# Performance work log

Measured on AMD Instinct MI355X. Metric: run time of the kernel, lower is better.

Reference implementation:

```python
import jax, jax.numpy as jnp
import numpy as np

T, H, I, E, K = 8192, 2048, 768, 16, 2  # tokens, hidden, moe_intermediate, experts, top_k


def setup_inputs() -> dict:
    key = jax.random.key(0)
    k0, k1, k2, k3, k4 = jax.random.split(key, 5)
    return {
        "hidden_states": jax.random.normal(k0, (T, H), jnp.float32),
        "top_k_index": jax.random.randint(k1, (T, K), 0, E),
        "top_k_weights": jax.random.uniform(k2, (T, K), jnp.float32),
        "gate_up_proj": jax.random.normal(k3, (E, 2 * I, H), jnp.float32) * 0.02,
        "down_proj": jax.random.normal(k4, (E, H, I), jnp.float32) * 0.02,
    }


def reference(hidden_states, top_k_index, top_k_weights, gate_up_proj, down_proj):
    num_experts = gate_up_proj.shape[0]
    # combine[t, e] = sum over k of top_k_weights[t, k] where top_k_index[t, k] == e
    # (duplicated expert picks sum their weights, matching torch index_add_ semantics)
    onehot = jax.nn.one_hot(top_k_index, num_experts, dtype=hidden_states.dtype)  # [T, K, E]
    combine = jnp.einsum("tke,tk->te", onehot, top_k_weights)                      # [T, E]
    out = jnp.zeros_like(hidden_states)
    # fixed small loop over structurally distinct experts; unselected tokens get weight 0
    for e in range(num_experts):
        gate_up = hidden_states @ gate_up_proj[e].T        # [T, 2I]
        gate, up = jnp.split(gate_up, 2, axis=-1)
        act = jax.nn.silu(gate) * up                       # SwiGLU, [T, I]
        down = act @ down_proj[e].T                        # [T, H]
        out = out + down * combine[:, e:e + 1]
    return out
```

## Files before the change

kernel.cpp:

```cpp
#include <hip/hip_runtime.h>

#define TT 8192
#define HH 2048
#define II 768
#define NE 16
#define TOPK 2
#define CAP 16384
#define BM 128

typedef float f32x4 __attribute__((ext_vector_type(4)));
typedef float f32x8 __attribute__((ext_vector_type(8)));
typedef short bf16x8 __attribute__((ext_vector_type(8)));
typedef unsigned short ushort8 __attribute__((ext_vector_type(8)));

__device__ __forceinline__ unsigned short f2bf(float f) {
    unsigned u = __builtin_bit_cast(unsigned, f);
    u += 0x7fffu + ((u >> 16) & 1u);
    return (unsigned short)(u >> 16);
}

__device__ __forceinline__ float bf2f(unsigned short u) {
    return __builtin_bit_cast(float, (unsigned)u << 16);
}

__device__ __forceinline__ void glds16(const void* g, void* l) {
    __builtin_amdgcn_global_load_lds((const __attribute__((address_space(1))) void*)g,
                                     (__attribute__((address_space(3))) void*)l, 16, 0, 0);
}

__global__ void cast_hs_kernel(const float* __restrict__ src, unsigned short* __restrict__ dst) {
    int i = blockIdx.x * blockDim.x + threadIdx.x;
    const float4 v = reinterpret_cast<const float4*>(src)[i];
    ushort4 o;
    o.x = f2bf(v.x); o.y = f2bf(v.y); o.z = f2bf(v.z); o.w = f2bf(v.w);
    reinterpret_cast<ushort4*>(dst)[i] = o;
}

__global__ void cast_w1_kernel(const float* __restrict__ gup, unsigned short* __restrict__ wg1) {
    size_t gid = (size_t)blockIdx.x * 256 + threadIdx.x;
    int sc = gid & 7;
    int r = (gid >> 3) & 255;
    int kt = (gid >> 11) & 31;
    int rest = (int)(gid >> 16);
    int it = rest % 6;
    int e = rest / 6;
    int chunk = sc ^ (r & 7);
    int grow = (r < 128) ? (it * 128 + r) : (II + it * 128 + (r - 128));
    const float4* s = reinterpret_cast<const float4*>(
        &gup[((size_t)e * (2 * II) + grow) * HH + kt * 64 + chunk * 8]);
    float4 v0 = s[0], v1 = s[1];
    ushort8 o;
    o[0] = f2bf(v0.x); o[1] = f2bf(v0.y); o[2] = f2bf(v0.z); o[3] = f2bf(v0.w);
    o[4] = f2bf(v1.x); o[5] = f2bf(v1.y); o[6] = f2bf(v1.z); o[7] = f2bf(v1.w);
    *reinterpret_cast<ushort8*>(&wg1[gid * 8]) = o;
}

__global__ void cast_w2_kernel(const float* __restrict__ dwn, unsigned short* __restrict__ wg2) {
    size_t gid = (size_t)blockIdx.x * 256 + threadIdx.x;
    int sc = gid & 7;
    int r = (gid >> 3) & 127;
    int kt = (int)((gid >> 10) % 12);
    int rest = (int)(gid / (12 << 10));
    int ht = rest & 15;
    int e = rest >> 4;
    int chunk = sc ^ (r & 7);
    int hrow = ht * 128 + r;
    const float4* s = reinterpret_cast<const float4*>(
        &dwn[((size_t)e * HH + hrow) * II + kt * 64 + chunk * 8]);
    float4 v0 = s[0], v1 = s[1];
    ushort8 o;
    o[0] = f2bf(v0.x); o[1] = f2bf(v0.y); o[2] = f2bf(v0.z); o[3] = f2bf(v0.w);
    o[4] = f2bf(v1.x); o[5] = f2bf(v1.y); o[6] = f2bf(v1.z); o[7] = f2bf(v1.w);
    *reinterpret_cast<ushort8*>(&wg2[gid * 8]) = o;
}

__global__ void route_kernel(const int* __restrict__ idx, const float* __restrict__ w,
                             int* __restrict__ counts, int* __restrict__ toks,
                             float* __restrict__ wts) {
    int t = blockIdx.x * blockDim.x + threadIdx.x;
    if (t >= TT) return;
    #pragma unroll
    for (int k = 0; k < TOPK; ++k) {
        int e = idx[t * TOPK + k];
        int p = atomicAdd(&counts[e], 1);
        toks[e * CAP + p] = t | (k << 15);
        wts[e * CAP + p] = w[t * TOPK + k];
    }
}

__global__ void scan_kernel(const int* __restrict__ counts, int* __restrict__ poffs,
                            int* __restrict__ ntot, int* __restrict__ tmap) {
    if (threadIdx.x == 0) {
        int s = 0, nt = 0;
        for (int e = 0; e < NE; ++e) {
            poffs[e] = s;
            int ct = (counts[e] + 127) >> 7;
            for (int m = 0; m < ct; ++m) tmap[nt++] = e | (m << 8);
            s += ct << 7;
        }
        poffs[NE] = s;
        ntot[0] = nt;
    }
}

__global__ __launch_bounds__(256, 2) void gemm1_kernel(
    const unsigned short* __restrict__ hsb, const unsigned short* __restrict__ wg1,
    const int* __restrict__ counts, const int* __restrict__ poffs,
    const int* __restrict__ ntotp, const int* __restrict__ tmap,
    const int* __restrict__ toks, unsigned short* __restrict__ actT) {
    const int b = blockIdx.x;
    const int w = (b & 7) * 108 + (b >> 3);
    const int ibt = w / 144;
    const int gt = w % 144;
    if (gt >= ntotp[0]) return;
    const int ent = tmap[gt];
    const int e = ent & 255;
    const int mbase = (ent >> 8) << 7;
    const int cnt = counts[e];
    const int tid = threadIdx.x;
    const int lane = tid & 63;
    const int wid = tid >> 6;
    const int wm = wid >> 1, wn = wid & 1;

    __shared__ unsigned short sA[128 * 64];
    __shared__ unsigned short sB[256 * 64];
    __shared__ int s_tok[BM];

    if (tid < BM) {
        int r = mbase + tid;
        s_tok[tid] = toks[e * CAP + ((r < cnt) ? r : (cnt - 1))] & 0x1FFF;
    }
    __syncthreads();

    size_t abase[4];
    #pragma unroll
    for (int it = 0; it < 4; ++it) {
        int idx = it * 256 + tid;
        int r = idx >> 3, sc = idx & 7;
        abase[it] = (size_t)s_tok[r] * HH + ((sc ^ (r & 7)) << 3);
    }
    const unsigned short* bbase = wg1 + ((size_t)(e * 6 + ibt) << 19) + (size_t)tid * 8;

    f32x4 accg[4][4], accu[4][4];
    #pragma unroll
    for (int m = 0; m < 4; ++m)
        #pragma unroll
        for (int n = 0; n < 4; ++n) {
            accg[m][n] = (f32x4){0.f, 0.f, 0.f, 0.f};
            accu[m][n] = (f32x4){0.f, 0.f, 0.f, 0.f};
        }

    const int lrow = lane & 15;
    const int lk8 = (lane >> 4) << 3;

    for (int k0 = 0; k0 < HH; k0 += 64) {
        #pragma unroll
        for (int it = 0; it < 4; ++it)
            glds16(hsb + abase[it] + k0, (char*)sA + it * 4096 + wid * 1024);
        const unsigned short* bk = bbase + ((size_t)(k0 >> 6) * 16384);
        #pragma unroll
        for (int it = 0; it < 8; ++it)
            glds16(bk + it * 2048, (char*)sB + it * 4096 + wid * 1024);
        __syncthreads();
        #pragma unroll
        for (int ks = 0; ks < 2; ++ks) {
            bf16x8 af[4], bg[4], bu[4];
            #pragma unroll
            for (int m = 0; m < 4; ++m) {
                int row = wm * 64 + m * 16 + lrow;
                af[m] = *reinterpret_cast<const bf16x8*>(
                    &sA[(row << 6) + ((ks * 32 + lk8) ^ ((row & 7) << 3))]);
            }
            #pragma unroll
            for (int n = 0; n < 4; ++n) {
                int rg = wn * 64 + n * 16 + lrow;
                bg[n] = *reinterpret_cast<const bf16x8*>(
                    &sB[(rg << 6) + ((ks * 32 + lk8) ^ ((rg & 7) << 3))]);
                int ru = rg + 128;
                bu[n] = *reinterpret_cast<const bf16x8*>(
                    &sB[(ru << 6) + ((ks * 32 + lk8) ^ ((ru & 7) << 3))]);
            }
            #pragma unroll
            for (int m = 0; m < 4; ++m)
                #pragma unroll
                for (int n = 0; n < 4; ++n) {
                    accg[m][n] = __builtin_amdgcn_mfma_f32_16x16x32_bf16(af[m], bg[n], accg[m][n], 0, 0, 0);
                    accu[m][n] = __builtin_amdgcn_mfma_f32_16x16x32_bf16(af[m], bu[n], accu[m][n], 0, 0, 0);
                }
        }
        __syncthreads();
    }

    const int mt = (poffs[e] + mbase) >> 7;
    #pragma unroll
    for (int m = 0; m < 4; ++m)
        #pragma unroll
        for (int n = 0; n < 4; ++n)
            #pragma unroll
            for (int j = 0; j < 4; ++j) {
                int row = wm * 64 + m * 16 + ((lane >> 4) << 2) + j;
                if (mbase + row < cnt) {
                    int c = wn * 64 + n * 16 + lrow;
                    int ktile = ibt * 2 + (c >> 6);
                    int cc = c & 63;
                    float g = accg[m][n][j], u = accu[m][n][j];
                    float a = (g / (1.f + __expf(-g))) * u;
                    actT[((size_t)(mt * 12 + ktile) * 128 + row) * 64 +
                         (((cc >> 3) ^ (row & 7)) << 3) + (cc & 7)] = f2bf(a);
                }
            }
}

__global__ __launch_bounds__(256) void gemm2_kernel(
    const unsigned short* __restrict__ actT, const unsigned short* __restrict__ wg2,
    const int* __restrict__ counts, const int* __restrict__ poffs,
    const int* __restrict__ ntotp, const int* __restrict__ tmap,
    const int* __restrict__ toks, const float* __restrict__ wts,
    unsigned short* __restrict__ partial) {
    const int b = blockIdx.x;
    const int w = (b & 7) * 288 + (b >> 3);
    const int ht = w / 144;
    const int gt = w % 144;
    if (gt >= ntotp[0]) return;
    const int ent = tmap[gt];
    const int e = ent & 255;
    const int mbase = (ent >> 8) << 7;
    const int cnt = counts[e];
    const int tid = threadIdx.x;
    const int lane = tid & 63;
    const int wid = tid >> 6;
    const int wm = wid >> 1, wn = wid & 1;

    __shared__ unsigned short sA[128 * 64];
    __shared__ unsigned short sB[128 * 64];
    __shared__ int s_tok[BM];
    __shared__ float s_wt[BM];

    if (tid < BM) {
        int r = mbase + tid;
        int rc = (r < cnt) ? r : (cnt - 1);
        s_tok[tid] = toks[e * CAP + rc];
        s_wt[tid] = wts[e * CAP + rc];
    }

    const int mt = (poffs[e] + mbase) >> 7;
    const unsigned short* abase = actT + (size_t)(mt * 12) * 8192 + (size_t)tid * 8;
    const unsigned short* bbase = wg2 + (size_t)((e * 16 + ht) * 12) * 8192 + (size_t)tid * 8;

    f32x4 acc[4][4];
    #pragma unroll
    for (int m = 0; m < 4; ++m)
        #pragma unroll
        for (int n = 0; n < 4; ++n) acc[m][n] = (f32x4){0.f, 0.f, 0.f, 0.f};

    const int lrow = lane & 15;
    const int lk8 = (lane >> 4) << 3;

    for (int kt = 0; kt < 12; ++kt) {
        #pragma unroll
        for (int it = 0; it < 4; ++it)
            glds16(abase + (size_t)kt * 8192 + it * 2048, (char*)sA + it * 4096 + wid * 1024);
        #pragma unroll
        for (int it = 0; it < 4; ++it)
            glds16(bbase + (size_t)kt * 8192 + it * 2048, (char*)sB + it * 4096 + wid * 1024);
        __syncthreads();
        #pragma unroll
        for (int ks = 0; ks < 2; ++ks) {
            bf16x8 af[4], bb[4];
            #pragma unroll
            for (int m = 0; m < 4; ++m) {
                int row = wm * 64 + m * 16 + lrow;
                af[m] = *reinterpret_cast<const bf16x8*>(
                    &sA[(row << 6) + ((ks * 32 + lk8) ^ ((row & 7) << 3))]);
            }
            #pragma unroll
            for (int n = 0; n < 4; ++n) {
                int rb = wn * 64 + n * 16 + lrow;
                bb[n] = *reinterpret_cast<const bf16x8*>(
                    &sB[(rb << 6) + ((ks * 32 + lk8) ^ ((rb & 7) << 3))]);
            }
            #pragma unroll
            for (int m = 0; m < 4; ++m)
                #pragma unroll
                for (int n = 0; n < 4; ++n)
                    acc[m][n] = __builtin_amdgcn_mfma_f32_16x16x32_bf16(af[m], bb[n], acc[m][n], 0, 0, 0);
        }
        __syncthreads();
    }

    #pragma unroll
    for (int m = 0; m < 4; ++m) {
        int row = wm * 64 + m * 16 + ((lane >> 4) << 2);
        #pragma unroll
        for (int j = 0; j < 4; ++j) {
            if (mbase + row + j < cnt) {
                int v = s_tok[row + j];
                size_t rbase = ((size_t)(v >> 15) * TT + (v & 0x1FFF)) * HH + ht * 128;
                float w = s_wt[row + j];
                #pragma unroll
                for (int n = 0; n < 4; ++n)
                    partial[rbase + wn * 64 + n * 16 + lrow] = f2bf(acc[m][n][j] * w);
            }
        }
    }
}

__global__ void combine_kernel(const unsigned short* __restrict__ partial, float* __restrict__ out) {
    size_t i = (size_t)blockIdx.x * blockDim.x + threadIdx.x;
    const ushort8 a = reinterpret_cast<const ushort8*>(partial)[i];
    const ushort8 b = reinterpret_cast<const ushort8*>(partial + (size_t)TT * HH)[i];
    f32x8 o;
    #pragma unroll
    for (int j = 0; j < 8; ++j) o[j] = bf2f(a[j]) + bf2f(b[j]);
    *reinterpret_cast<f32x8*>(&out[i * 8]) = o;
}

extern "C" void kernel_launch(void* const* d_in, const int* in_sizes, int n_in,
                              void* d_out, int out_size, void* d_ws, size_t ws_size,
                              hipStream_t stream) {
    const float* hs = (const float*)d_in[0];
    const int* tki = (const int*)d_in[1];
    const float* tkw = (const float*)d_in[2];
    const float* gup = (const float*)d_in[3];
    const float* dwn = (const float*)d_in[4];
    float* out = (float*)d_out;

    char* ws = (char*)d_ws;
    int* counts = (int*)(ws);
    int* poffs = (int*)(ws + 128);
    int* ntot = (int*)(ws + 224);
    int* tmap = (int*)(ws + 256);
    int* toks = (int*)(ws + 1024);
    float* wts = (float*)(ws + 1024 + (size_t)CAP * NE * 4);
    unsigned short* hsb = (unsigned short*)(ws + 2098176);
    unsigned short* wg1 = (unsigned short*)(ws + 35652608);
    unsigned short* wg2 = (unsigned short*)(ws + 136315904);
    unsigned short* actT = (unsigned short*)(ws + 186647552);
    unsigned short* partial = (unsigned short*)(ws + 2098176);

    hipMemsetAsync(counts, 0, 1024, stream);
    route_kernel<<<TT / 256, 256, 0, stream>>>(tki, tkw, counts, toks, wts);
    scan_kernel<<<1, 64, 0, stream>>>(counts, poffs, ntot, tmap);
    cast_hs_kernel<<<(TT * HH / 4) / 256, 256, 0, stream>>>(hs, hsb);
    cast_w1_kernel<<<24576, 256, 0, stream>>>(gup, wg1);
    cast_w2_kernel<<<12288, 256, 0, stream>>>(dwn, wg2);
    gemm1_kernel<<<864, 256, 0, stream>>>(hsb, wg1, counts, poffs, ntot, tmap, toks, actT);
    gemm2_kernel<<<2304, 256, 0, stream>>>(actT, wg2, counts, poffs, ntot, tmap, toks, wts, partial);
    combine_kernel<<<(TT * HH / 8) / 256, 256, 0, stream>>>(partial, out);
}
```

Before: 394.5 us.

## Double-buffer LDS tiles in both MoE GEMM kernels to overlap loads with MFMA

Both grouped GEMM kernels now use ping-pong shared-memory buffers, issuing the async global-to-LDS loads for the next K tile before computing on the current one. This cuts the per-iteration barrier count from two to one and hides load latency behind MFMA work. The launch-bounds occupancy hint moves from gemm1 to gemm2. gemm1's LDS use doubles to about 96KB, which likely allows only one block per CU and may cost latency hiding across waves.

Result: slower. 482.2 us (+22.2%).

```diff
diff --git a/kernel.cpp b/kernel.cpp
--- a/kernel.cpp
+++ b/kernel.cpp
@@ -103,7 +103,7 @@
     }
 }
 
-__global__ __launch_bounds__(256, 2) void gemm1_kernel(
+__global__ __launch_bounds__(256) void gemm1_kernel(
     const unsigned short* __restrict__ hsb, const unsigned short* __restrict__ wg1,
     const int* __restrict__ counts, const int* __restrict__ poffs,
     const int* __restrict__ ntotp, const int* __restrict__ tmap,
@@ -122,8 +122,8 @@
     const int wid = tid >> 6;
     const int wm = wid >> 1, wn = wid & 1;
 
-    __shared__ unsigned short sA[128 * 64];
-    __shared__ unsigned short sB[256 * 64];
+    __shared__ unsigned short sA0[128 * 64], sA1[128 * 64];
+    __shared__ unsigned short sB0[256 * 64], sB1[256 * 64];
     __shared__ int s_tok[BM];
 
     if (tid < BM) {
@@ -153,43 +153,62 @@
     const int lrow = lane & 15;
     const int lk8 = (lane >> 4) << 3;
 
-    for (int k0 = 0; k0 < HH; k0 += 64) {
-        #pragma unroll
-        for (int it = 0; it < 4; ++it)
-            glds16(hsb + abase[it] + k0, (char*)sA + it * 4096 + wid * 1024);
-        const unsigned short* bk = bbase + ((size_t)(k0 >> 6) * 16384);
-        #pragma unroll
-        for (int it = 0; it < 8; ++it)
-            glds16(bk + it * 2048, (char*)sB + it * 4096 + wid * 1024);
+#define G1_STAGE(SA, SB, kt) do {                                              \
+    _Pragma("unroll")                                                          \
+    for (int it = 0; it < 4; ++it)                                             \
+        glds16(hsb + abase[it] + (size_t)(kt) * 64,                            \
+               (char*)(SA) + it * 4096 + wid * 1024);                          \
+    const unsigned short* bk_ = bbase + (size_t)(kt) * 16384;                  \
+    _Pragma("unroll")                                                          \
+    for (int it = 0; it < 8; ++it)                                             \
+        glds16(bk_ + it * 2048, (char*)(SB) + it * 4096 + wid * 1024);         \
+} while (0)
+
+#define G1_COMPUTE(SA, SB) do {                                                \
+    _Pragma("unroll")                                                          \
+    for (int ks = 0; ks < 2; ++ks) {                                           \
+        bf16x8 af[4], bg[4], bu[4];                                            \
+        _Pragma("unroll")                                                      \
+        for (int m = 0; m < 4; ++m) {                                          \
+            int row = wm * 64 + m * 16 + lrow;                                 \
+            af[m] = *reinterpret_cast<const bf16x8*>(                          \
+                &(SA)[(row << 6) + ((ks * 32 + lk8) ^ ((row & 7) << 3))]);     \
+        }                                                                      \
+        _Pragma("unroll")                                                      \
+        for (int n = 0; n < 4; ++n) {                                          \
+            int rg = wn * 64 + n * 16 + lrow;                                  \
+            bg[n] = *reinterpret_cast<const bf16x8*>(                          \
+                &(SB)[(rg << 6) + ((ks * 32 + lk8) ^ ((rg & 7) << 3))]);       \
+            int ru = rg + 128;                                                 \
+            bu[n] = *reinterpret_cast<const bf16x8*>(                          \
+                &(SB)[(ru << 6) + ((ks * 32 + lk8) ^ ((ru & 7) << 3))]);       \
+        }                                                                      \
+        _Pragma("unroll")                                                      \
+        for (int m = 0; m < 4; ++m)                                            \
+            _Pragma("unroll")                                                  \
+            for (int n = 0; n < 4; ++n) {                                      \
+                accg[m][n] = __builtin_amdgcn_mfma_f32_16x16x32_bf16(          \
+                    af[m], bg[n], accg[m][n], 0, 0, 0);                        \
+                accu[m][n] = __builtin_amdgcn_mfma_f32_16x16x32_bf16(          \
+                    af[m], bu[n], accu[m][n], 0, 0, 0);                        \
+            }                                                                  \
+    }                                                                          \
+} while (0)
+
+    G1_STAGE(sA0, sB0, 0);
+    __syncthreads();
+    for (int kt = 0; kt < 30; kt += 2) {
+        G1_STAGE(sA1, sB1, kt + 1);
+        G1_COMPUTE(sA0, sB0);
         __syncthreads();
-        #pragma unroll
-        for (int ks = 0; ks < 2; ++ks) {
-            bf16x8 af[4], bg[4], bu[4];
-            #pragma unroll
-            for (int m = 0; m < 4; ++m) {
-                int row = wm * 64 + m * 16 + lrow;
-                af[m] = *reinterpret_cast<const bf16x8*>(
-                    &sA[(row << 6) + ((ks * 32 + lk8) ^ ((row & 7) << 3))]);
-            }
-            #pragma unroll
-            for (int n = 0; n < 4; ++n) {
-                int rg = wn * 64 + n * 16 + lrow;
-                bg[n] = *reinterpret_cast<const bf16x8*>(
-                    &sB[(rg << 6) + ((ks * 32 + lk8) ^ ((rg & 7) << 3))]);
-                int ru = rg + 128;
-                bu[n] = *reinterpret_cast<const bf16x8*>(
-                    &sB[(ru << 6) + ((ks * 32 + lk8) ^ ((ru & 7) << 3))]);
-            }
-            #pragma unroll
-            for (int m = 0; m < 4; ++m)
-                #pragma unroll
-                for (int n = 0; n < 4; ++n) {
-                    accg[m][n] = __builtin_amdgcn_mfma_f32_16x16x32_bf16(af[m], bg[n], accg[m][n], 0, 0, 0);
-                    accu[m][n] = __builtin_amdgcn_mfma_f32_16x16x32_bf16(af[m], bu[n], accu[m][n], 0, 0, 0);
-                }
-        }
+        G1_STAGE(sA0, sB0, kt + 2);
+        G1_COMPUTE(sA1, sB1);
         __syncthreads();
     }
+    G1_STAGE(sA1, sB1, 31);
+    G1_COMPUTE(sA0, sB0);
+    __syncthreads();
+    G1_COMPUTE(sA1, sB1);
 
     const int mt = (poffs[e] + mbase) >> 7;
     #pragma unroll
@@ -211,7 +230,7 @@
             }
 }
 
-__global__ __launch_bounds__(256) void gemm2_kernel(
+__global__ __launch_bounds__(256, 2) void gemm2_kernel(
     const unsigned short* __restrict__ actT, const unsigned short* __restrict__ wg2,
     const int* __restrict__ counts, const int* __restrict__ poffs,
     const int* __restrict__ ntotp, const int* __restrict__ tmap,
@@ -231,8 +250,8 @@
     const int wid = tid >> 6;
     const int wm = wid >> 1, wn = wid & 1;
 
-    __shared__ unsigned short sA[128 * 64];
-    __shared__ unsigned short sB[128 * 64];
+    __shared__ unsigned short sA0[128 * 64], sA1[128 * 64];
+    __shared__ unsigned short sB0[128 * 64], sB1[128 * 64];
     __shared__ int s_tok[BM];
     __shared__ float s_wt[BM];
 
@@ -256,37 +275,56 @@
     const int lrow = lane & 15;
     const int lk8 = (lane >> 4) << 3;
 
-    for (int kt = 0; kt < 12; ++kt) {
-        #pragma unroll
-        for (int it = 0; it < 4; ++it)
-            glds16(abase + (size_t)kt * 8192 + it * 2048, (char*)sA + it * 4096 + wid * 1024);
-        #pragma unroll
-        for (int it = 0; it < 4; ++it)
-            glds16(bbase + (size_t)kt * 8192 + it * 2048, (char*)sB + it * 4096 + wid * 1024);
+#define G2_STAGE(SA, SB, kt) do {                                              \
+    _Pragma("unroll")                                                          \
+    for (int it = 0; it < 4; ++it)                                             \
+        glds16(abase + (size_t)(kt) * 8192 + it * 2048,                        \
+               (char*)(SA) + it * 4096 + wid * 1024);                          \
+    _Pragma("unroll")                                                          \
+    for (int it = 0; it < 4; ++it)                                             \
+        glds16(bbase + (size_t)(kt) * 8192 + it * 2048,                        \
+               (char*)(SB) + it * 4096 + wid * 1024);                          \
+} while (0)
+
+#define G2_COMPUTE(SA, SB) do {                                                \
+    _Pragma("unroll")                                                          \
+    for (int ks = 0; ks < 2; ++ks) {                                           \
+        bf16x8 af[4], bb[4];                                                   \
+        _Pragma("unroll")                                                      \
+        for (int m = 0; m < 4; ++m) {                                          \
+            int row = wm * 64 + m * 16 + lrow;                                 \
+            af[m] = *reinterpret_cast<const bf16x8*>(                          \
+                &(SA)[(row << 6) + ((ks * 32 + lk8) ^ ((row & 7) << 3))]);     \
+        }                                                                      \
+        _Pragma("unroll")                                                      \
+        for (int n = 0; n < 4; ++n) {                                          \
+            int rb = wn * 64 + n * 16 + lrow;                                  \
+            bb[n] = *reinterpret_cast<const bf16x8*>(                          \
+                &(SB)[(rb << 6) + ((ks * 32 + lk8) ^ ((rb & 7) << 3))]);       \
+        }                                                                      \
+        _Pragma("unroll")                                                      \
+        for (int m = 0; m < 4; ++m)                                            \
+            _Pragma("unroll")                                                  \
+            for (int n = 0; n < 4; ++n)                                        \
+                acc[m][n] = __builtin_amdgcn_mfma_f32_16x16x32_bf16(           \
+                    af[m], bb[n], acc[m][n], 0, 0, 0);                         \
+    }                                                                          \
+} while (0)
+
+    G2_STAGE(sA0, sB0, 0);
+    __syncthreads();
+    for (int kt = 0; kt < 10; kt += 2) {
+        G2_STAGE(sA1, sB1, kt + 1);
+        G2_COMPUTE(sA0, sB0);
         __syncthreads();
-        #pragma unroll
-        for (int ks = 0; ks < 2; ++ks) {
-            bf16x8 af[4], bb[4];
-            #pragma unroll
-            for (int m = 0; m < 4; ++m) {
-                int row = wm * 64 + m * 16 + lrow;
-                af[m] = *reinterpret_cast<const bf16x8*>(
-                    &sA[(row << 6) + ((ks * 32 + lk8) ^ ((row & 7) << 3))]);
-            }
-            #pragma unroll
-            for (int n = 0; n < 4; ++n) {
-                int rb = wn * 64 + n * 16 + lrow;
-                bb[n] = *reinterpret_cast<const bf16x8*>(
-                    &sB[(rb << 6) + ((ks * 32 + lk8) ^ ((rb & 7) << 3))]);
-            }
-            #pragma unroll
-            for (int m = 0; m < 4; ++m)
-                #pragma unroll
-                for (int n = 0; n < 4; ++n)
-                    acc[m][n] = __builtin_amdgcn_mfma_f32_16x16x32_bf16(af[m], bb[n], acc[m][n], 0, 0, 0);
-        }
+        G2_STAGE(sA0, sB0, kt + 2);
+        G2_COMPUTE(sA1, sB1);
         __syncthreads();
     }
+    G2_STAGE(sA1, sB1, 11);
+    G2_COMPUTE(sA0, sB0);
+    __syncthreads();
+    G2_COMPUTE(sA1, sB1);
 
     #pragma unroll
     for (int m = 0; m < 4; ++m) {
```
